# Optimization experiments

Hardware: AMD Instinct MI355X
Metric: run time of the kernel (lower is better)

The kernel has to match this reference:

```python
import jax, jax.numpy as jnp
import numpy as np

NUM_RBF = 16
TOP_K = 30
NUM_POS_EMB = 16
EDGE_FEATURES = 128
MAX_REL_POS = 32  # ProteinMPNN max_relative_feature


def _rbf(D):
    # D: [...,]; returns [..., NUM_RBF]
    D_min, D_max = 2.0, 22.0
    D_mu = jnp.linspace(D_min, D_max, NUM_RBF)
    D_sigma = (D_max - D_min) / NUM_RBF
    return jnp.exp(-((D[..., None] - D_mu) / D_sigma) ** 2)


def _dist(Xca, mask, eps=1e-6):
    # Xca: [B,L,3], mask: [B,L]
    mask_2D = mask[:, :, None] * mask[:, None, :]  # [B,L,L]
    dX = Xca[:, :, None, :] - Xca[:, None, :, :]
    D = mask_2D * jnp.sqrt(jnp.sum(dX * dX, -1) + eps)
    D_max = jnp.max(D, -1, keepdims=True)
    D_adjust = D + (1.0 - mask_2D) * D_max
    L = Xca.shape[1]
    k = min(TOP_K, L)
    neg_topk, E_idx = jax.lax.top_k(-D_adjust, k)  # smallest distances
    return -neg_topk, E_idx  # D_neighbors:[B,L,K], E_idx:[B,L,K] int32


def _gather_nodes_pair(A, E_idx):
    # A: [B,L], E_idx: [B,L,K] -> [B,L,K]
    return jnp.take_along_axis(A[:, None, :].repeat(A.shape[1], 1), E_idx, axis=2)


def _rbf_pair(A, B_, E_idx):
    # A,B_: [B,L,3]; distances from A[i] to B_[j] for j in neighbors of i
    Bn = jnp.take_along_axis(B_[:, None, :, :].repeat(B_.shape[1], 1), E_idx[..., None].repeat(3, -1), axis=2)  # [B,L,K,3]
    D = jnp.sqrt(jnp.sum((A[:, :, None, :] - Bn) ** 2, -1) + 1e-6)
    return _rbf(D)


def setup_inputs() -> dict:
    key = jax.random.key(0)
    k1, k2, k3, k4 = jax.random.split(key, 4)
    B, L = 8, 2048
    X = jax.random.normal(k1, (B, L, 4, 3), dtype=jnp.float32) * 5.0
    mask = jnp.ones((B, L), dtype=jnp.float32)
    residue_idx = jnp.broadcast_to(jnp.arange(L, dtype=jnp.int32), (B, L))
    chain_labels = jnp.zeros((B, L), dtype=jnp.int32)
    in_dim = NUM_POS_EMB + NUM_RBF * 25  # 16 + 400 = 416
    W_e = jax.random.normal(k2, (in_dim, EDGE_FEATURES), dtype=jnp.float32) * (1.0 / np.sqrt(in_dim))
    b_e = jnp.zeros((EDGE_FEATURES,), dtype=jnp.float32)
    g_e = jnp.ones((EDGE_FEATURES,), dtype=jnp.float32)  # layernorm gamma
    be_ln = jnp.zeros((EDGE_FEATURES,), dtype=jnp.float32)  # layernorm beta
    pe_dim = 2 * MAX_REL_POS + 2  # 66
    W_pe = jax.random.normal(k3, (pe_dim, NUM_POS_EMB), dtype=jnp.float32) * (1.0 / np.sqrt(pe_dim))
    b_pe = jnp.zeros((NUM_POS_EMB,), dtype=jnp.float32)
    return {"X": X, "mask": mask, "residue_idx": residue_idx, "chain_labels": chain_labels,
            "W_e": W_e, "b_e": b_e, "g_e": g_e, "be_ln": be_ln, "W_pe": W_pe, "b_pe": b_pe}


def reference(X, mask, residue_idx, chain_labels, W_e, b_e, g_e, be_ln, W_pe, b_pe):
    # atoms
    N = X[:, :, 0, :]
    Ca = X[:, :, 1, :]
    C = X[:, :, 2, :]
    O = X[:, :, 3, :]
    # virtual Cb (ProteinMPNN formula)
    b = Ca - N
    c = C - Ca
    a = jnp.cross(b, c)
    Cb = -0.58273431 * a + 0.56802827 * b - 0.54067466 * c + Ca

    D_neighbors, E_idx = _dist(Ca, mask)

    atoms = {"N": N, "Ca": Ca, "C": C, "O": O, "Cb": Cb}
    order = ["Ca", "N", "C", "O", "Cb"]
    rbf_list = []
    for ai in order:
        for aj in order:
            if ai == "Ca" and aj == "Ca":
                rbf_list.append(_rbf(D_neighbors))
            else:
                rbf_list.append(_rbf_pair(atoms[ai], atoms[aj], E_idx))
    RBF_all = jnp.concatenate(rbf_list, axis=-1)  # [B,L,K,400]

    # positional encodings (ProteinMPNN style)
    offset = residue_idx[:, :, None] - residue_idx[:, None, :]  # [B,L,L]
    offset = jnp.take_along_axis(offset, E_idx, axis=2)  # [B,L,K]
    d_chains = (chain_labels[:, :, None] == chain_labels[:, None, :]).astype(jnp.int32)
    E_chains = jnp.take_along_axis(d_chains, E_idx, axis=2)  # [B,L,K]
    d = jnp.clip(offset + MAX_REL_POS, 0, 2 * MAX_REL_POS) * E_chains + (1 - E_chains) * (2 * MAX_REL_POS + 1)
    d_onehot = jax.nn.one_hot(d, 2 * MAX_REL_POS + 2, dtype=RBF_all.dtype)
    E_pos = d_onehot @ W_pe + b_pe  # [B,L,K,16]

    E = jnp.concatenate([E_pos, RBF_all], axis=-1)  # [B,L,K,416]
    E = E @ W_e + b_e  # [B,L,K,128]
    # layer norm
    mu = jnp.mean(E, -1, keepdims=True)
    var = jnp.var(E, -1, keepdims=True)
    E = (E - mu) / jnp.sqrt(var + 1e-5) * g_e + be_ln
    return E, E_idx
```

## Files before the change

### kernel.cpp

```cpp
#include <hip/hip_runtime.h>
#include <hip/hip_bf16.h>
#include <stdint.h>

#define BB   8
#define LL   2048
#define KK   30
#define COUT 128
#define FIN  416
#define PE_DIM 16
#define MAXREL 32
#define KSTEPS 26
#define WTILES (KSTEPS * 4)

typedef __attribute__((ext_vector_type(8)))  short short8;
typedef __attribute__((ext_vector_type(4)))  float f32x4;
typedef __attribute__((ext_vector_type(16))) float f32x16;

__device__ __forceinline__ unsigned int f2bf(float x) {
    unsigned int u = __float_as_uint(x);
    return (u + 0x7fffu + ((u >> 16) & 1u)) >> 16;
}

__device__ __forceinline__ unsigned int packbf2(float a, float b) {
    float2 f; f.x = a; f.y = b;
    __hip_bfloat162 h = __float22bfloat162_rn(f);
    unsigned int u;
    __builtin_memcpy(&u, &h, 4);
    return u;
}

__device__ __forceinline__ short8 as_s8(uint4 u) {
    union { uint4 u; short8 s; } x; x.u = u; return x.s;
}

__device__ __forceinline__ int lanes_below(unsigned long long m) {
    return __builtin_amdgcn_mbcnt_hi((unsigned)(m >> 32),
           __builtin_amdgcn_mbcnt_lo((unsigned)m, 0));
}

__global__ __launch_bounds__(256)
void atoms_kernel(const float* __restrict__ X, float4* __restrict__ atoms4) {
    int idx = blockIdx.x * 256 + threadIdx.x;
    if (idx >= BB * LL) return;
    int b = idx >> 11;
    int i = idx & (LL - 1);
    const float4* xp = reinterpret_cast<const float4*>(X + (size_t)idx * 12);
    float4 p0 = xp[0], p1 = xp[1], p2 = xp[2];
    float Nx = p0.x, Ny = p0.y, Nz = p0.z;
    float Ax = p0.w, Ay = p1.x, Az = p1.y;
    float Cx = p1.z, Cy = p1.w, Cz = p2.x;
    float Ox = p2.y, Oy = p2.z, Oz = p2.w;
    float bx = Ax - Nx, by = Ay - Ny, bz = Az - Nz;
    float cx = Cx - Ax, cy = Cy - Ay, cz = Cz - Az;
    float ax = by * cz - bz * cy;
    float ay = bz * cx - bx * cz;
    float az = bx * cy - by * cx;
    float Cbx = -0.58273431f * ax + 0.56802827f * bx - 0.54067466f * cx + Ax;
    float Cby = -0.58273431f * ay + 0.56802827f * by - 0.54067466f * cy + Ay;
    float Cbz = -0.58273431f * az + 0.56802827f * bz - 0.54067466f * cz + Az;
    float4* ab = atoms4 + (size_t)b * 5 * LL;
    ab[0 * LL + i] = make_float4(Ax, Ay, Az, 0.f);
    ab[1 * LL + i] = make_float4(Nx, Ny, Nz, 0.f);
    ab[2 * LL + i] = make_float4(Cx, Cy, Cz, 0.f);
    ab[3 * LL + i] = make_float4(Ox, Oy, Oz, 0.f);
    ab[4 * LL + i] = make_float4(Cbx, Cby, Cbz, 0.f);
}

__global__ __launch_bounds__(256)
void wfrag_kernel(const float* __restrict__ W_e, unsigned short* __restrict__ wf) {
    int idx = blockIdx.x * 256 + threadIdx.x;
    if (idx >= WTILES * 64) return;
    int lane = idx & 63;
    int tile = idx >> 6;
    int ks = tile >> 2, nt = tile & 3;
    int n  = nt * 32 + (lane & 31);
    int kb = ks * 16 + (lane >> 5) * 8;
    unsigned int p[8];
    #pragma unroll
    for (int j = 0; j < 8; j++) p[j] = f2bf(W_e[(size_t)(kb + j) * COUT + n]);
    uint4 w;
    w.x = p[0] | (p[1] << 16);
    w.y = p[2] | (p[3] << 16);
    w.z = p[4] | (p[5] << 16);
    w.w = p[6] | (p[7] << 16);
    reinterpret_cast<uint4*>(wf)[idx] = w;
}

__global__ __launch_bounds__(256)
void topk_kernel(const float4* __restrict__ atoms4, unsigned short* __restrict__ eidx,
                 float* __restrict__ out_eidx_f) {
    __shared__ unsigned long long skeys[4][32];
    int t = threadIdx.x;
    int wv = t >> 6, ln = t & 63;
    int row = blockIdx.x * 4 + wv;
    int b = row >> 11, i = row & (LL - 1);
    const float4* cab = atoms4 + (size_t)b * 5 * LL;
    float4 pi = cab[i];
    float xi = pi.x, yi = pi.y, zi = pi.z;
    unsigned int bits[32];
    unsigned int mn = 0xffffffffu, lmx = 0u;
    #pragma unroll
    for (int r = 0; r < 32; r++) {
        int j = ln + 64 * r;
        float4 pj = cab[j];
        float dx = __fsub_rn(xi, pj.x);
        float dy = __fsub_rn(yi, pj.y);
        float dz = __fsub_rn(zi, pj.z);
        float s = __fadd_rn(__fadd_rn(__fmul_rn(dx, dx), __fmul_rn(dy, dy)),
                            __fmul_rn(dz, dz));
        s = __fadd_rn(s, 1e-6f);
        float D = __fsqrt_rn(s);
        unsigned int ub = __float_as_uint(D);
        bits[r] = ub;
        mn  = mn  < ub ? mn  : ub;
        lmx = lmx > ub ? lmx : ub;
    }
    #pragma unroll
    for (int off = 1; off < 64; off <<= 1) {
        unsigned int om = __shfl_xor(mn, off);
        unsigned int ox = __shfl_xor(lmx, off);
        mn  = mn  < om ? mn  : om;
        lmx = lmx < ox ? lmx : ox;
    }
    unsigned int lo = __builtin_amdgcn_readfirstlane(mn);
    unsigned int hi = __builtin_amdgcn_readfirstlane(lmx);

    while (lo < hi) {
        unsigned int mid = lo + ((hi - lo) >> 1);
        int c = 0;
        #pragma unroll
        for (int r = 0; r < 32; r++)
            c += __popcll(__ballot(bits[r] <= mid));
        if (c >= KK) hi = mid; else lo = mid + 1;
    }
    unsigned int T = lo;

    int clt = 0;
    #pragma unroll
    for (int r = 0; r < 32; r++)
        clt += __popcll(__ballot(bits[r] < T));
    int need_ties = KK - clt;

    int base = 0, tiebase = 0;
    #pragma unroll
    for (int r = 0; r < 32; r++) {
        bool lt = bits[r] < T;
        bool eq = bits[r] == T;
        unsigned long long bq = __ballot(eq);
        int trk = tiebase + lanes_below(bq);
        bool sel = lt || (eq && trk < need_ties);
        unsigned long long bs = __ballot(sel);
        int pos = base + lanes_below(bs);
        if (sel)
            skeys[wv][pos] = ((unsigned long long)bits[r] << 11) |
                             (unsigned long long)(unsigned)(ln + 64 * r);
        base    += __popcll(bs);
        tiebase += __popcll(bq);
    }
    asm volatile("s_waitcnt lgkmcnt(0)" ::: "memory");

    unsigned long long mykey = (ln < KK) ? skeys[wv][ln] : ~0ull;
    int rank = 0;
    for (int s = 0; s < KK; s++) {
        unsigned long long other = __shfl(mykey, s);
        rank += (other < mykey) ? 1 : 0;
    }
    if (ln < KK) {
        int jw = (int)(mykey & 2047ull);
        eidx[(size_t)row * KK + rank] = (unsigned short)jw;
        out_eidx_f[(size_t)row * KK + rank] = (float)jw;
    }
}

__global__ __launch_bounds__(256)
void edge_kernel(const float4* __restrict__ atoms4, const unsigned short* __restrict__ eidx,
                 const int* __restrict__ residx, const int* __restrict__ chains,
                 const float* __restrict__ W_pe, const float* __restrict__ b_pe,
                 const unsigned short* __restrict__ wfrag,
                 const float* __restrict__ b_e,  const float* __restrict__ g_e,
                 const float* __restrict__ be_ln, float* __restrict__ outE) {
    __shared__ float d25L[4][32][26];
    int t = threadIdx.x;
    int w = t >> 6, l = t & 63;
    int e32 = l & 31, half = l >> 5;
    int ebase = blockIdx.x * 128;
    int b0 = ebase / (LL * KK);
    int e0 = ebase + w * 32;

    int eL  = e0 + e32;
    int biL = eL / KK;
    int i2L = biL & (LL - 1);
    int jv  = eidx[eL];
    int offv  = residx[biL] - residx[(b0 << 11) + jv];
    int samev = (chains[biL] == chains[(b0 << 11) + jv]);
    int dd = offv + MAXREL;
    dd = dd < 0 ? 0 : (dd > 2 * MAXREL ? 2 * MAXREL : dd);
    int dsl = samev ? dd : (2 * MAXREL + 1);

    const float4* ap = atoms4 + (size_t)b0 * 5 * LL;

    #pragma unroll
    for (int rr = 0; rr < 13; rr++) {
        int task = rr * 64 + l;
        if (task < 800) {
            int p  = task >> 5, el = task & 31;
            int ai = (p * 205) >> 10;
            int aj = p - ai * 5;
            int i2 = __shfl(i2L, el);
            int j2 = __shfl(jv,  el);
            float4 A  = ap[(size_t)ai * LL + i2];
            float4 Bv = ap[(size_t)aj * LL + j2];
            float dx = A.x - Bv.x, dy = A.y - Bv.y, dz = A.z - Bv.z;
            d25L[w][el][p] = __builtin_amdgcn_sqrtf(dx * dx + dy * dy + dz * dz + 1e-6f);
        }
    }
    asm volatile("s_waitcnt lgkmcnt(0)" ::: "memory");

    const float QQ = 0.10273981f;
    float mu_a = half ? 18.0f : 7.3333333f;

    f32x16 acc[4];
    #pragma unroll
    for (int nt = 0; nt < 4; nt++)
        #pragma unroll
        for (int r = 0; r < 16; r++) acc[nt][r] = 0.f;

    const uint4* Bg = reinterpret_cast<const uint4*>(wfrag);
    #pragma unroll
    for (int ks = 0; ks < KSTEPS; ks++) {
        uint4 bu0 = Bg[((size_t)(ks * 4 + 0)) * 64 + l];
        uint4 bu1 = Bg[((size_t)(ks * 4 + 1)) * 64 + l];
        uint4 bu2 = Bg[((size_t)(ks * 4 + 2)) * 64 + l];
        uint4 bu3 = Bg[((size_t)(ks * 4 + 3)) * 64 + l];

        float v[8];
        if (ks == 0) {
            const float4* wp4 = reinterpret_cast<const float4*>(W_pe + dsl * PE_DIM + half * 8);
            const float4* bp4 = reinterpret_cast<const float4*>(b_pe + half * 8);
            float4 wa = wp4[0], wb = wp4[1];
            float4 ba = bp4[0], bb = bp4[1];
            v[0] = wa.x + ba.x; v[1] = wa.y + ba.y; v[2] = wa.z + ba.z; v[3] = wa.w + ba.w;
            v[4] = wb.x + bb.x; v[5] = wb.y + bb.y; v[6] = wb.z + bb.z; v[7] = wb.w + bb.w;
        } else {
            float d = d25L[w][e32][ks - 1];
            float t4 = fminf(d - mu_a, 50.0f);
            float e4 = __builtin_amdgcn_exp2f(-0.92332483f * (t4 * t4));
            float g  = __builtin_amdgcn_exp2f(__builtin_fmaf(2.4621995f, t4, -1.6414664f));
            float u  = QQ * __builtin_amdgcn_rcpf(g);
            v[4] = e4;
            float e = e4, r = g;
            e *= r; v[5] = e; r *= QQ; e *= r; v[6] = e; r *= QQ; e *= r; v[7] = e;
            e = e4; r = u;
            e *= r; v[3] = e; r *= QQ; e *= r; v[2] = e; r *= QQ; e *= r; v[1] = e;
            r *= QQ; e *= r; v[0] = e;
        }
        uint4 pk;
        pk.x = packbf2(v[0], v[1]);
        pk.y = packbf2(v[2], v[3]);
        pk.z = packbf2(v[4], v[5]);
        pk.w = packbf2(v[6], v[7]);
        short8 afrag = as_s8(pk);
        acc[0] = __builtin_amdgcn_mfma_f32_32x32x16_bf16(afrag, as_s8(bu0), acc[0], 0, 0, 0);
        acc[1] = __builtin_amdgcn_mfma_f32_32x32x16_bf16(afrag, as_s8(bu1), acc[1], 0, 0, 0);
        acc[2] = __builtin_amdgcn_mfma_f32_32x32x16_bf16(afrag, as_s8(bu2), acc[2], 0, 0, 0);
        acc[3] = __builtin_amdgcn_mfma_f32_32x32x16_bf16(afrag, as_s8(bu3), acc[3], 0, 0, 0);
    }

    float be_[4], ge_[4], bl_[4];
    #pragma unroll
    for (int nt = 0; nt < 4; nt++) {
        be_[nt] = b_e[nt * 32 + e32];
        ge_[nt] = g_e[nt * 32 + e32];
        bl_[nt] = be_ln[nt * 32 + e32];
    }

    #pragma unroll
    for (int reg = 0; reg < 16; reg++) {
        float vv[4];
        float s = 0.f, s2 = 0.f;
        #pragma unroll
        for (int nt = 0; nt < 4; nt++) {
            float x = acc[nt][reg] + be_[nt];
            vv[nt] = x;
            s += x; s2 += x * x;
        }
        #pragma unroll
        for (int off = 1; off < 32; off <<= 1) {
            s  += __shfl_xor(s,  off);
            s2 += __shfl_xor(s2, off);
        }
        float mu  = s * (1.0f / 128.0f);
        float var = s2 * (1.0f / 128.0f) - mu * mu;
        float rs  = rsqrtf(var + 1e-5f);
        int e = e0 + (reg & 3) + 8 * (reg >> 2) + 4 * half;
        float* op = outE + (size_t)e * COUT + e32;
        #pragma unroll
        for (int nt = 0; nt < 4; nt++)
            op[nt * 32] = (vv[nt] - mu) * rs * ge_[nt] + bl_[nt];
    }
}

extern "C" void kernel_launch(void* const* d_in, const int* in_sizes, int n_in,
                              void* d_out, int out_size, void* d_ws, size_t ws_size,
                              hipStream_t stream) {
    const float* X      = (const float*)d_in[0];
    const int*   residx = (const int*)d_in[2];
    const int*   chains = (const int*)d_in[3];
    const float* W_e    = (const float*)d_in[4];
    const float* b_e    = (const float*)d_in[5];
    const float* g_e    = (const float*)d_in[6];
    const float* be_ln  = (const float*)d_in[7];
    const float* W_pe   = (const float*)d_in[8];
    const float* b_pe   = (const float*)d_in[9];

    float* outE     = (float*)d_out;
    float* outEidxF = outE + (size_t)BB * LL * KK * COUT;

    float4*         atoms4 = (float4*)d_ws;
    unsigned short* eidx   = (unsigned short*)(atoms4 + (size_t)BB * 5 * LL);
    unsigned short* wf     = eidx + (size_t)BB * LL * KK;

    atoms_kernel<<<(BB * LL + 255) / 256, 256, 0, stream>>>(X, atoms4);
    wfrag_kernel<<<(WTILES * 64 + 255) / 256, 256, 0, stream>>>(W_e, wf);
    topk_kernel <<<BB * LL / 4, 256, 0, stream>>>(atoms4, eidx, outEidxF);
    edge_kernel <<<(BB * LL * KK) / 128, 256, 0, stream>>>(
        atoms4, eidx, residx, chains, W_pe, b_pe, wf, b_e, g_e, be_ln, outE);
}
```

Baseline: 436.7 us.

## Split edge GEMM K dimension across wave pairs and prefetch weight fragments

Each 256-thread block now handles 64 edges instead of 128, with two waves per 32-edge group. Each wave of a pair computes half the 26 K-steps and half of the 25 pairwise distances, and the partial MFMA accumulators are combined through shared memory before layernorm. Weight fragment loads are also software-prefetched one K-step ahead. The aim is to shorten each wave's serial MFMA/exp chain and raise parallelism, at the cost of twice as many blocks, a __syncthreads, 16KB of extra LDS traffic for the reduction, and half the waves idling during the epilogue.

```diff
diff --git a/kernel.cpp b/kernel.cpp
--- a/kernel.cpp
+++ b/kernel.cpp
@@ -10,6 +10,7 @@
 #define PE_DIM 16
 #define MAXREL 32
 #define KSTEPS 26
+#define KHALF  13
 #define WTILES (KSTEPS * 4)
 
 typedef __attribute__((ext_vector_type(8)))  short short8;
@@ -179,13 +180,15 @@
                  const unsigned short* __restrict__ wfrag,
                  const float* __restrict__ b_e,  const float* __restrict__ g_e,
                  const float* __restrict__ be_ln, float* __restrict__ outE) {
-    __shared__ float d25L[4][32][26];
+    __shared__ float  d25L[2][32][26];
+    __shared__ float4 cmb[2][4][4][64];
     int t = threadIdx.x;
     int w = t >> 6, l = t & 63;
+    int g = w >> 1, kh = w & 1;
     int e32 = l & 31, half = l >> 5;
-    int ebase = blockIdx.x * 128;
+    int ebase = blockIdx.x * 64;
     int b0 = ebase / (LL * KK);
-    int e0 = ebase + w * 32;
+    int e0 = ebase + g * 32;
 
     int eL  = e0 + e32;
     int biL = eL / KK;
@@ -199,10 +202,10 @@
 
     const float4* ap = atoms4 + (size_t)b0 * 5 * LL;
 
-    #pragma unroll
-    for (int rr = 0; rr < 13; rr++) {
-        int task = rr * 64 + l;
-        if (task < 800) {
+    if (kh == 0) {
+        #pragma unroll
+        for (int rr = 0; rr < 6; rr++) {
+            int task = rr * 64 + l;
             int p  = task >> 5, el = task & 31;
             int ai = (p * 205) >> 10;
             int aj = p - ai * 5;
@@ -211,7 +214,23 @@
             float4 A  = ap[(size_t)ai * LL + i2];
             float4 Bv = ap[(size_t)aj * LL + j2];
             float dx = A.x - Bv.x, dy = A.y - Bv.y, dz = A.z - Bv.z;
-            d25L[w][el][p] = __builtin_amdgcn_sqrtf(dx * dx + dy * dy + dz * dz + 1e-6f);
+            d25L[g][el][p] = __builtin_amdgcn_sqrtf(dx * dx + dy * dy + dz * dz + 1e-6f);
+        }
+    } else {
+        #pragma unroll
+        for (int rr = 0; rr < 7; rr++) {
+            int task = rr * 64 + l;
+            if (task < 416) {
+                int p  = 12 + (task >> 5), el = task & 31;
+                int ai = (p * 205) >> 10;
+                int aj = p - ai * 5;
+                int i2 = __shfl(i2L, el);
+                int j2 = __shfl(jv,  el);
+                float4 A  = ap[(size_t)ai * LL + i2];
+                float4 Bv = ap[(size_t)aj * LL + j2];
+                float dx = A.x - Bv.x, dy = A.y - Bv.y, dz = A.z - Bv.z;
+                d25L[g][el][p] = __builtin_amdgcn_sqrtf(dx * dx + dy * dy + dz * dz + 1e-6f);
+            }
         }
     }
     asm volatile("s_waitcnt lgkmcnt(0)" ::: "memory");
@@ -226,15 +245,25 @@
         for (int r = 0; r < 16; r++) acc[nt][r] = 0.f;
 
     const uint4* Bg = reinterpret_cast<const uint4*>(wfrag);
-    #pragma unroll
-    for (int ks = 0; ks < KSTEPS; ks++) {
-        uint4 bu0 = Bg[((size_t)(ks * 4 + 0)) * 64 + l];
-        uint4 bu1 = Bg[((size_t)(ks * 4 + 1)) * 64 + l];
-        uint4 bu2 = Bg[((size_t)(ks * 4 + 2)) * 64 + l];
-        uint4 bu3 = Bg[((size_t)(ks * 4 + 3)) * 64 + l];
-
+    int ksb = kh * KHALF;
+
+    uint4 cb0 = Bg[((size_t)((ksb) * 4 + 0)) * 64 + l];
+    uint4 cb1 = Bg[((size_t)((ksb) * 4 + 1)) * 64 + l];
+    uint4 cb2 = Bg[((size_t)((ksb) * 4 + 2)) * 64 + l];
+    uint4 cb3 = Bg[((size_t)((ksb) * 4 + 3)) * 64 + l];
+
+    #pragma unroll
+    for (int kk = 0; kk < KHALF; kk++) {
+        int ks = ksb + kk;
+        uint4 nb0, nb1, nb2, nb3;
+        if (kk + 1 < KHALF) {
+            nb0 = Bg[((size_t)((ks + 1) * 4 + 0)) * 64 + l];
+            nb1 = Bg[((size_t)((ks + 1) * 4 + 1)) * 64 + l];
+            nb2 = Bg[((size_t)((ks + 1) * 4 + 2)) * 64 + l];
+            nb3 = Bg[((size_t)((ks + 1) * 4 + 3)) * 64 + l];
+        }
         float v[8];
-        if (ks == 0) {
+        if (kh == 0 && kk == 0) {
             const float4* wp4 = reinterpret_cast<const float4*>(W_pe + dsl * PE_DIM + half * 8);
             const float4* bp4 = reinterpret_cast<const float4*>(b_pe + half * 8);
             float4 wa = wp4[0], wb = wp4[1];
@@ -242,13 +271,13 @@
             v[0] = wa.x + ba.x; v[1] = wa.y + ba.y; v[2] = wa.z + ba.z; v[3] = wa.w + ba.w;
             v[4] = wb.x + bb.x; v[5] = wb.y + bb.y; v[6] = wb.z + bb.z; v[7] = wb.w + bb.w;
         } else {
-            float d = d25L[w][e32][ks - 1];
+            float d = d25L[g][e32][ks - 1];
             float t4 = fminf(d - mu_a, 50.0f);
             float e4 = __builtin_amdgcn_exp2f(-0.92332483f * (t4 * t4));
-            float g  = __builtin_amdgcn_exp2f(__builtin_fmaf(2.4621995f, t4, -1.6414664f));
-            float u  = QQ * __builtin_amdgcn_rcpf(g);
+            float gg = __builtin_amdgcn_exp2f(__builtin_fmaf(2.4621995f, t4, -1.6414664f));
+            float u  = QQ * __builtin_amdgcn_rcpf(gg);
             v[4] = e4;
-            float e = e4, r = g;
+            float e = e4, r = gg;
             e *= r; v[5] = e; r *= QQ; e *= r; v[6] = e; r *= QQ; e *= r; v[7] = e;
             e = e4; r = u;
             e *= r; v[3] = e; r *= QQ; e *= r; v[2] = e; r *= QQ; e *= r; v[1] = e;
@@ -260,11 +289,34 @@
         pk.z = packbf2(v[4], v[5]);
         pk.w = packbf2(v[6], v[7]);
         short8 afrag = as_s8(pk);
-        acc[0] = __builtin_amdgcn_mfma_f32_32x32x16_bf16(afrag, as_s8(bu0), acc[0], 0, 0, 0);
-        acc[1] = __builtin_amdgcn_mfma_f32_32x32x16_bf16(afrag, as_s8(bu1), acc[1], 0, 0, 0);
-        acc[2] = __builtin_amdgcn_mfma_f32_32x32x16_bf16(afrag, as_s8(bu2), acc[2], 0, 0, 0);
-        acc[3] = __builtin_amdgcn_mfma_f32_32x32x16_bf16(afrag, as_s8(bu3), acc[3], 0, 0, 0);
-    }
+        acc[0] = __builtin_amdgcn_mfma_f32_32x32x16_bf16(afrag, as_s8(cb0), acc[0], 0, 0, 0);
+        acc[1] = __builtin_amdgcn_mfma_f32_32x32x16_bf16(afrag, as_s8(cb1), acc[1], 0, 0, 0);
+        acc[2] = __builtin_amdgcn_mfma_f32_32x32x16_bf16(afrag, as_s8(cb2), acc[2], 0, 0, 0);
+        acc[3] = __builtin_amdgcn_mfma_f32_32x32x16_bf16(afrag, as_s8(cb3), acc[3], 0, 0, 0);
+        if (kk + 1 < KHALF) { cb0 = nb0; cb1 = nb1; cb2 = nb2; cb3 = nb3; }
+    }
+
+    if (kh == 1) {
+        #pragma unroll
+        for (int nt = 0; nt < 4; nt++)
+            #pragma unroll
+            for (int r4 = 0; r4 < 4; r4++)
+                cmb[g][nt][r4][l] = make_float4(acc[nt][4 * r4 + 0], acc[nt][4 * r4 + 1],
+                                                acc[nt][4 * r4 + 2], acc[nt][4 * r4 + 3]);
+    }
+    __syncthreads();
+    if (kh == 1) return;
+
+    #pragma unroll
+    for (int nt = 0; nt < 4; nt++)
+        #pragma unroll
+        for (int r4 = 0; r4 < 4; r4++) {
+            float4 c4 = cmb[g][nt][r4][l];
+            acc[nt][4 * r4 + 0] += c4.x;
+            acc[nt][4 * r4 + 1] += c4.y;
+            acc[nt][4 * r4 + 2] += c4.z;
+            acc[nt][4 * r4 + 3] += c4.w;
+        }
 
     float be_[4], ge_[4], bl_[4];
     #pragma unroll
@@ -323,6 +375,6 @@
     atoms_kernel<<<(BB * LL + 255) / 256, 256, 0, stream>>>(X, atoms4);
     wfrag_kernel<<<(WTILES * 64 + 255) / 256, 256, 0, stream>>>(W_e, wf);
     topk_kernel <<<BB * LL / 4, 256, 0, stream>>>(atoms4, eidx, outEidxF);
-    edge_kernel <<<(BB * LL * KK) / 128, 256, 0, stream>>>(
+    edge_kernel <<<(BB * LL * KK) / 64, 256, 0, stream>>>(
         atoms4, eidx, residx, chains, W_pe, b_pe, wf, b_e, g_e, be_ln, outE);
 }
```

After: 452.4 us. 3.6% more time.
